# Performance work log

Hardware: AMD Instinct MI355X
Metric: run time of the kernel (lower is better)

Reference implementation:

```python
import jax, jax.numpy as jnp
import numpy as np

N_HEAD = 12
N_EMBD = 768


def setup_inputs() -> dict:
    key = jax.random.key(0)
    k1, k2, k3, k4, k5 = jax.random.split(key, 5)
    B, T, C = 4, 2048, N_EMBD
    s = 0.02
    x = jax.random.normal(k1, (B, T, C), dtype=jnp.float32)
    w_attn = jax.random.normal(k2, (C, 3 * C), dtype=jnp.float32) * s
    b_attn = jnp.zeros((3 * C,), dtype=jnp.float32)
    w_proj = jax.random.normal(k3, (C, C), dtype=jnp.float32) * s
    b_proj = jnp.zeros((C,), dtype=jnp.float32)
    return {"x": x, "w_attn": w_attn, "b_attn": b_attn, "w_proj": w_proj, "b_proj": b_proj}


def reference(x, w_attn, b_attn, w_proj, b_proj):
    # dropout omitted (eval mode / dropout=0.0)
    B, T, C = x.shape
    H = N_HEAD
    D = C // H  # head dim
    qkv = x @ w_attn + b_attn                      # [B,T,3C]
    q, k, v = jnp.split(qkv, 3, axis=-1)
    q = q.reshape(B, T, H, D).transpose(0, 2, 1, 3)  # [B,H,T,D]
    k = k.reshape(B, T, H, D).transpose(0, 2, 1, 3)
    v = v.reshape(B, T, H, D).transpose(0, 2, 1, 3)
    att = jnp.einsum('bhqd,bhkd->bhqk', q, k) * (1.0 / np.sqrt(D))  # [B,H,T,T]
    causal = jnp.tril(jnp.ones((T, T), dtype=bool))
    att = jnp.where(causal[None, None], att, -jnp.inf)
    att = jax.nn.softmax(att, axis=-1)
    y = jnp.einsum('bhqk,bhkd->bhqd', att, v)      # [B,H,T,D]
    y = y.transpose(0, 2, 1, 3).reshape(B, T, C)
    return y @ w_proj + b_proj
```

## Files before the change

### kernel.cpp

```cpp
#include <hip/hip_runtime.h>
#include <stdint.h>

typedef unsigned short ushort_t;

#define T_SEQ 2048
#define BATCH 4
#define NHEAD 12
#define CEMB 768
#define HDIM 64
#define C3 2304

__device__ __forceinline__ ushort_t f2b_hw(float f) {
  union { __bf16 h; ushort_t u; } p;
  p.h = (__bf16)f;
  return p.u;
}
__device__ __forceinline__ uint32_t pkbf16(float lo, float hi) {
  union { __bf16 h[2]; uint32_t u; } p;
  p.h[0] = (__bf16)lo; p.h[1] = (__bf16)hi;
  return p.u;
}

typedef __attribute__((address_space(3))) unsigned int lds_u32_t;
typedef const __attribute__((address_space(1))) unsigned int glb_u32_t;
__device__ __forceinline__ void async_cp16(const void* g, void* l) {
  __builtin_amdgcn_global_load_lds((glb_u32_t*)g, (lds_u32_t*)l, 16, 0, 0);
}

__global__ __launch_bounds__(256) void prep_k(const float* __restrict__ x, ushort_t* __restrict__ xb,
                                              const float* __restrict__ wa, ushort_t* __restrict__ wT,
                                              const float* __restrict__ wp, ushort_t* __restrict__ wpT) {
  const int blk = blockIdx.x;
  const int tid = threadIdx.x;
  if (blk < 3072) {
    const int i = blk * 256 + tid;
    float4 a = ((const float4*)x)[2 * i];
    float4 b = ((const float4*)x)[2 * i + 1];
    uint4 v;
    v.x = pkbf16(a.x, a.y); v.y = pkbf16(a.z, a.w);
    v.z = pkbf16(b.x, b.y); v.w = pkbf16(b.z, b.w);
    ((uint4*)xb)[i] = v;
    return;
  }
  __shared__ ushort_t tile[32][33];
  const float* in; ushort_t* out; int R, C, bx, by;
  if (blk < 4800) {
    const int t = blk - 3072;
    in = wa; out = wT; R = CEMB; C = C3;
    bx = t % 72; by = t / 72;
  } else {
    const int t = blk - 4800;
    in = wp; out = wpT; R = CEMB; C = CEMB;
    bx = t % 24; by = t / 24;
  }
  const int tx = tid & 31, ty = tid >> 5;
  const int c0 = bx * 32, r0 = by * 32;
  for (int i = ty; i < 32; i += 8)
    tile[i][tx] = f2b_hw(in[(size_t)(r0 + i) * C + c0 + tx]);
  __syncthreads();
  for (int i = ty; i < 32; i += 8)
    out[(size_t)(c0 + i) * R + r0 + tx] = tile[tx][i];
}

typedef __bf16 bf16x8 __attribute__((ext_vector_type(8)));
typedef float f32x4 __attribute__((ext_vector_type(4)));

template <bool OUTF, int BM>
__global__ __launch_bounds__(256) void gemm_bt(const ushort_t* __restrict__ A,
                                               const ushort_t* __restrict__ Bt,
                                               const float* __restrict__ bias,
                                               void* __restrict__ Cv,
                                               int M, int N, int K) {
  constexpr int TM = BM / 32;
  __shared__ ushort_t As[2 * BM * 32];
  __shared__ ushort_t Bs[2 * 128 * 32];
  const int tid = threadIdx.x;
  const int m0 = blockIdx.y * BM, n0 = blockIdx.x * 128;
  const int wid = tid >> 6, lane = tid & 63;
  const int quad = lane >> 4, l15 = lane & 15;
  const int wm = (wid >> 1) * (BM / 2), wn = (wid & 1) * 64;
  f32x4 acc[TM][4] = {};

  const int e0 = tid * 8;
  const int r0s = e0 >> 5, c0s = e0 & 31;
  const int e1 = e0 + 2048;
  const int r1s = e1 >> 5, c1s = e1 & 31;

  for (int k0 = 0; k0 < K; k0 += 64) {
    __syncthreads();
#pragma unroll
    for (int p = 0; p < 2; p++) {
      const int kc = k0 + p * 32;
      async_cp16(&A[(size_t)(m0 + r0s) * K + kc + c0s], &As[p * BM * 32 + e0]);
      if constexpr (BM == 128)
        async_cp16(&A[(size_t)(m0 + r1s) * K + kc + c1s], &As[p * BM * 32 + e1]);
      async_cp16(&Bt[(size_t)(n0 + r0s) * K + kc + c0s], &Bs[p * 128 * 32 + e0]);
      async_cp16(&Bt[(size_t)(n0 + r1s) * K + kc + c1s], &Bs[p * 128 * 32 + e1]);
    }
    __syncthreads();
    bf16x8 af[TM][2], bfr[4][2];
#pragma unroll
    for (int t = 0; t < TM; t++)
#pragma unroll
      for (int p = 0; p < 2; p++)
        af[t][p] = *(const bf16x8*)&As[p * BM * 32 + (wm + t * 16 + l15) * 32 + quad * 8];
#pragma unroll
    for (int t = 0; t < 4; t++)
#pragma unroll
      for (int p = 0; p < 2; p++)
        bfr[t][p] = *(const bf16x8*)&Bs[p * 128 * 32 + (wn + t * 16 + l15) * 32 + quad * 8];
#pragma unroll
    for (int p = 0; p < 2; p++)
#pragma unroll
      for (int tm = 0; tm < TM; tm++)
#pragma unroll
        for (int tn = 0; tn < 4; tn++)
          acc[tm][tn] = __builtin_amdgcn_mfma_f32_16x16x32_bf16(af[tm][p], bfr[tn][p], acc[tm][tn], 0, 0, 0);
  }

#pragma unroll
  for (int tm = 0; tm < TM; tm++) {
    const int row = m0 + wm + tm * 16 + quad * 4;
#pragma unroll
    for (int tn = 0; tn < 4; tn++) {
      const int col = n0 + wn + tn * 16 + l15;
      const float bv = bias[col];
#pragma unroll
      for (int rr = 0; rr < 4; rr++) {
        if constexpr (OUTF)
          ((float*)Cv)[(size_t)(row + rr) * N + col] = acc[tm][tn][rr] + bv;
        else
          ((ushort_t*)Cv)[(size_t)(row + rr) * N + col] = f2b_hw(acc[tm][tn][rr] + bv);
      }
    }
  }
}

#define VSTR 64

__device__ __forceinline__ void commit_v(ushort_t* __restrict__ vt, const int* __restrict__ offs,
                                         uint4 pV0, uint4 pV1) {
  union { uint32_t u[4]; uint4 v; } a, c;
  a.v = pV0; c.v = pV1;
#pragma unroll
  for (int j = 0; j < 8; j++) {
    uint32_t pk = __builtin_amdgcn_perm(c.u[j >> 1], a.u[j >> 1],
                                        (j & 1) ? 0x07060302u : 0x05040100u);
    *(uint32_t*)&vt[offs[j]] = pk;
  }
}

__global__ __launch_bounds__(256, 3) void attn_mfma_k(const ushort_t* __restrict__ qkv,
                                                      ushort_t* __restrict__ y) {
  __shared__ ushort_t Ksm[2][2][64 * 32];
  __shared__ ushort_t Vt[2][64 * VSTR];
  __shared__ ushort_t Plds[4][32 * VSTR];

  const int qt = 15 - blockIdx.y;
  const int h = blockIdx.x >> 2, b = blockIdx.x & 3;
  const int tid = threadIdx.x;
  const int w = tid >> 6, lane = tid & 63;
  const int quad = lane >> 4, l15 = lane & 15;
  const int nkt = 2 * qt + 2;
  const int qw = qt * 128 + w * 32;

  const int e0 = tid * 8;
  const int kchunk = (tid & 3) ^ ((tid >> 3) & 3);
  const ushort_t* kbase = qkv + ((size_t)(b * T_SEQ) + (tid >> 2)) * C3 + CEMB + h * HDIM + kchunk * 8;
  const int vpair = tid & 31, vd0 = (tid >> 5) * 8;
  const ushort_t* vbase = qkv + ((size_t)(b * T_SEQ) + 2 * vpair) * C3 + 2 * CEMB + h * HDIM + vd0;
  const size_t step = (size_t)64 * C3;

  int voffw[8];
#pragma unroll
  for (int j = 0; j < 8; j++)
    voffw[j] = (vd0 + j) * VSTR + (((vpair >> 2) ^ j) << 3) + ((vpair & 3) << 1);

  const int sw7 = l15 & 7;
  int koff[4];
#pragma unroll
  for (int m = 0; m < 4; m++)
    koff[m] = (m * 16 + l15) * 32 + ((quad ^ ((l15 >> 1) & 3)) << 3);
  int vroff[2];
#pragma unroll
  for (int kb = 0; kb < 2; kb++)
    vroff[kb] = l15 * VSTR + (((quad + 4 * kb) ^ sw7) << 3);
  int poffW[2][4];
#pragma unroll
  for (int qf = 0; qf < 2; qf++)
#pragma unroll
    for (int m = 0; m < 4; m++)
      poffW[qf][m] = (qf * 16 + l15) * VSTR + (((2 * m + (quad >> 1)) ^ sw7) << 3) + ((quad & 1) << 2);

  const int qrel0 = w * 32 + l15;
  const int qrel1 = qrel0 + 16;

  const float C2 = 0.18033688011112042f;

  bf16x8 qB[2][2];
#pragma unroll
  for (int qf = 0; qf < 2; qf++)
#pragma unroll
    for (int kb = 0; kb < 2; kb++)
      qB[qf][kb] = *(const bf16x8*)&qkv[((size_t)(b * T_SEQ + qw + qf * 16 + l15)) * C3 +
                                        h * HDIM + kb * 32 + quad * 8];

  f32x4 o2[2][4] = {};
  float m0 = -3e38f, m1 = -3e38f;
  float lq0 = 0.f, lq1 = 0.f;

  const ushort_t* kp = kbase;
  const ushort_t* vp = vbase;
  uint4 pV0 = *(const uint4*)vp, pV1 = *(const uint4*)(vp + C3);
  async_cp16(kp, &Ksm[0][0][e0]);
  async_cp16(kp + 32, &Ksm[0][1][e0]);
  commit_v(Vt[0], voffw, pV0, pV1);
  vp += step;
  pV0 = *(const uint4*)vp; pV1 = *(const uint4*)(vp + C3);

  for (int kt = 0; kt < nkt; ++kt) {
    __syncthreads();
    if (kt + 1 < nkt) {
      const int nb = (kt + 1) & 1;
      kp += step;
      async_cp16(kp, &Ksm[nb][0][e0]);
      async_cp16(kp + 32, &Ksm[nb][1][e0]);
      commit_v(Vt[nb], voffw, pV0, pV1);
      if (kt + 2 < nkt) {
        vp += step;
        pV0 = *(const uint4*)vp; pV1 = *(const uint4*)(vp + C3);
      }
    }
    const int cb = kt & 1;

    bf16x8 kA[4][2];
#pragma unroll
    for (int m = 0; m < 4; m++) {
      kA[m][0] = *(const bf16x8*)&Ksm[cb][0][koff[m]];
      kA[m][1] = *(const bf16x8*)&Ksm[cb][1][koff[m]];
    }
    f32x4 st0[4] = {}, st1[4] = {};
#pragma unroll
    for (int m = 0; m < 4; m++) {
      st0[m] = __builtin_amdgcn_mfma_f32_16x16x32_bf16(kA[m][0], qB[0][0], st0[m], 0, 0, 0);
      st0[m] = __builtin_amdgcn_mfma_f32_16x16x32_bf16(kA[m][1], qB[0][1], st0[m], 0, 0, 0);
      st1[m] = __builtin_amdgcn_mfma_f32_16x16x32_bf16(kA[m][0], qB[1][0], st1[m], 0, 0, 0);
      st1[m] = __builtin_amdgcn_mfma_f32_16x16x32_bf16(kA[m][1], qB[1][1], st1[m], 0, 0, 0);
    }

    if (kt >= nkt - 2) {
      const int krel = (kt << 6) - (qt << 7) + quad * 4;
#pragma unroll
      for (int m = 0; m < 4; m++)
#pragma unroll
        for (int r = 0; r < 4; r++) {
          const int kr = krel + m * 16 + r;
          if (kr > qrel0) st0[m][r] = -3e38f;
          if (kr > qrel1) st1[m][r] = -3e38f;
        }
    }

    f32x4 mq0, mq1;
#pragma unroll
    for (int r = 0; r < 4; r++) {
      mq0[r] = fmaxf(fmaxf(st0[0][r], st0[1][r]), fmaxf(st0[2][r], st0[3][r]));
      mq1[r] = fmaxf(fmaxf(st1[0][r], st1[1][r]), fmaxf(st1[2][r], st1[3][r]));
    }
    const float mx0 = fmaxf(fmaxf(mq0[0], mq0[1]), fmaxf(mq0[2], mq0[3]));
    const float mx1 = fmaxf(fmaxf(mq1[0], mq1[1]), fmaxf(mq1[2], mq1[3]));

    float al0 = 1.f, al1 = 1.f;
    const bool viol = (mx0 - m0 > 22.18f) || (mx1 - m1 > 22.18f);
    if (__any(viol)) {
      float a = fmaxf(mx0, __shfl_xor(mx0, 16, 64));
      a = fmaxf(a, __shfl_xor(a, 32, 64));
      float bm = fmaxf(mx1, __shfl_xor(mx1, 16, 64));
      bm = fmaxf(bm, __shfl_xor(bm, 32, 64));
      const float n0 = fmaxf(m0, a), n1 = fmaxf(m1, bm);
      al0 = exp2f((m0 - n0) * C2);
      al1 = exp2f((m1 - n1) * C2);
      m0 = n0; m1 = n1;
#pragma unroll
      for (int nd = 0; nd < 4; nd++)
#pragma unroll
        for (int r = 0; r < 4; r++) {
          o2[0][nd][r] *= al0;
          o2[1][nd][r] *= al1;
        }
    }
    const float mnc0 = m0 * C2, mnc1 = m1 * C2;
#pragma unroll
    for (int m = 0; m < 4; m++)
#pragma unroll
      for (int r = 0; r < 4; r++) {
        st0[m][r] = exp2f(fmaf(st0[m][r], C2, -mnc0));
        st1[m][r] = exp2f(fmaf(st1[m][r], C2, -mnc1));
      }
    f32x4 s40, s41;
#pragma unroll
    for (int r = 0; r < 4; r++) {
      s40[r] = (st0[0][r] + st0[1][r]) + (st0[2][r] + st0[3][r]);
      s41[r] = (st1[0][r] + st1[1][r]) + (st1[2][r] + st1[3][r]);
    }
    lq0 = fmaf(lq0, al0, (s40[0] + s40[1]) + (s40[2] + s40[3]));
    lq1 = fmaf(lq1, al1, (s41[0] + s41[1]) + (s41[2] + s41[3]));

#pragma unroll
    for (int m = 0; m < 4; m++) {
      uint2 pk0, pk1;
      pk0.x = pkbf16(st0[m][0], st0[m][1]);
      pk0.y = pkbf16(st0[m][2], st0[m][3]);
      pk1.x = pkbf16(st1[m][0], st1[m][1]);
      pk1.y = pkbf16(st1[m][2], st1[m][3]);
      *(uint2*)&Plds[w][poffW[0][m]] = pk0;
      *(uint2*)&Plds[w][poffW[1][m]] = pk1;
    }

    asm volatile("s_waitcnt lgkmcnt(0)" ::: "memory");

    bf16x8 ap0[2], ap1[2], bvf[4][2];
#pragma unroll
    for (int kb = 0; kb < 2; kb++) {
      ap0[kb] = *(const bf16x8*)&Plds[w][vroff[kb]];
      ap1[kb] = *(const bf16x8*)&Plds[w][vroff[kb] + 16 * VSTR];
    }
#pragma unroll
    for (int nd = 0; nd < 4; nd++)
#pragma unroll
      for (int kb = 0; kb < 2; kb++)
        bvf[nd][kb] = *(const bf16x8*)&Vt[cb][nd * 1024 + vroff[kb]];
#pragma unroll
    for (int nd = 0; nd < 4; nd++) {
      o2[0][nd] = __builtin_amdgcn_mfma_f32_16x16x32_bf16(bvf[nd][0], ap0[0], o2[0][nd], 0, 0, 0);
      o2[0][nd] = __builtin_amdgcn_mfma_f32_16x16x32_bf16(bvf[nd][1], ap0[1], o2[0][nd], 0, 0, 0);
      o2[1][nd] = __builtin_amdgcn_mfma_f32_16x16x32_bf16(bvf[nd][0], ap1[0], o2[1][nd], 0, 0, 0);
      o2[1][nd] = __builtin_amdgcn_mfma_f32_16x16x32_bf16(bvf[nd][1], ap1[1], o2[1][nd], 0, 0, 0);
    }
  }

  {
    float lt0 = lq0 + __shfl_xor(lq0, 16, 64);
    lt0 += __shfl_xor(lt0, 32, 64);
    float lt1 = lq1 + __shfl_xor(lq1, 16, 64);
    lt1 += __shfl_xor(lt1, 32, 64);
    const float inv0 = 1.0f / lt0, inv1 = 1.0f / lt1;
#pragma unroll
    for (int qf = 0; qf < 2; qf++) {
      const float inv = qf ? inv1 : inv0;
      const int qg = qw + qf * 16 + l15;
      ushort_t* yp = y + ((size_t)(b * T_SEQ + qg)) * CEMB + h * HDIM + quad * 4;
#pragma unroll
      for (int nd = 0; nd < 4; nd++) {
        uint2 pk;
        pk.x = pkbf16(o2[qf][nd][0] * inv, o2[qf][nd][1] * inv);
        pk.y = pkbf16(o2[qf][nd][2] * inv, o2[qf][nd][3] * inv);
        *(uint2*)(yp + nd * 16) = pk;
      }
    }
  }
}

extern "C" void kernel_launch(void* const* d_in, const int* in_sizes, int n_in,
                              void* d_out, int out_size, void* d_ws, size_t ws_size,
                              hipStream_t stream) {
  const float* x      = (const float*)d_in[0];
  const float* w_attn = (const float*)d_in[1];
  const float* b_attn = (const float*)d_in[2];
  const float* w_proj = (const float*)d_in[3];
  const float* b_proj = (const float*)d_in[4];
  float* out = (float*)d_out;

  char* ws = (char*)d_ws;
  ushort_t* qkv = (ushort_t*)ws;
  ushort_t* y   = qkv + (size_t)8192 * 2304;
  ushort_t* xb  = y + (size_t)8192 * 768;
  ushort_t* wT  = xb + (size_t)8192 * 768;
  ushort_t* wpT = wT + (size_t)2304 * 768;

  prep_k<<<5376, 256, 0, stream>>>(x, xb, w_attn, wT, w_proj, wpT);

  gemm_bt<false, 128><<<dim3(C3 / 128, 8192 / 128), 256, 0, stream>>>(xb, wT, b_attn, qkv, 8192, C3, CEMB);

  attn_mfma_k<<<dim3(48, 16), 256, 0, stream>>>(qkv, y);

  gemm_bt<true, 64><<<dim3(CEMB / 128, 8192 / 64), 256, 0, stream>>>(y, wpT, b_proj, out, 8192, CEMB, CEMB);
}
```

Before: 215.9 us.

## Feed P directly from registers into 16x16x16 MFMA, drop P LDS round-trip

Removes the per-wave Plds shared buffer. The softmax probabilities are now packed into bf16 register fragments that already match the B-operand layout of the 16x16x16 MFMA, so they feed the PV product directly with no LDS store, wait and reload. The PV product now issues twice as many smaller MFMAs using 4-element V loads. The change also raises the occupancy hint from 3 to 4 blocks and interleaves query-tile order so heavy and light causal tiles alternate. The trade-off is more MFMA instructions, which have lower per-instruction throughput, and more register pressure under the tighter launch bound.

```diff
diff --git a/kernel.cpp b/kernel.cpp
--- a/kernel.cpp
+++ b/kernel.cpp
@@ -64,6 +64,7 @@
 
 typedef __bf16 bf16x8 __attribute__((ext_vector_type(8)));
 typedef float f32x4 __attribute__((ext_vector_type(4)));
+typedef short short4_t __attribute__((ext_vector_type(4)));
 
 template <bool OUTF, int BM>
 __global__ __launch_bounds__(256) void gemm_bt(const ushort_t* __restrict__ A,
@@ -150,13 +151,13 @@
   }
 }
 
-__global__ __launch_bounds__(256, 3) void attn_mfma_k(const ushort_t* __restrict__ qkv,
+__global__ __launch_bounds__(256, 4) void attn_mfma_k(const ushort_t* __restrict__ qkv,
                                                       ushort_t* __restrict__ y) {
   __shared__ ushort_t Ksm[2][2][64 * 32];
   __shared__ ushort_t Vt[2][64 * VSTR];
-  __shared__ ushort_t Plds[4][32 * VSTR];
-
-  const int qt = 15 - blockIdx.y;
+
+  const int by = blockIdx.y;
+  const int qt = (by & 1) ? (by >> 1) : (15 - (by >> 1));
   const int h = blockIdx.x >> 2, b = blockIdx.x & 3;
   const int tid = threadIdx.x;
   const int w = tid >> 6, lane = tid & 63;
@@ -181,16 +182,13 @@
 #pragma unroll
   for (int m = 0; m < 4; m++)
     koff[m] = (m * 16 + l15) * 32 + ((quad ^ ((l15 >> 1) & 3)) << 3);
-  int vroff[2];
-#pragma unroll
-  for (int kb = 0; kb < 2; kb++)
-    vroff[kb] = l15 * VSTR + (((quad + 4 * kb) ^ sw7) << 3);
-  int poffW[2][4];
-#pragma unroll
-  for (int qf = 0; qf < 2; qf++)
-#pragma unroll
-    for (int m = 0; m < 4; m++)
-      poffW[qf][m] = (qf * 16 + l15) * VSTR + (((2 * m + (quad >> 1)) ^ sw7) << 3) + ((quad & 1) << 2);
+  int vbrow[4], vcm[4];
+#pragma unroll
+  for (int nd = 0; nd < 4; nd++)
+    vbrow[nd] = (nd * 16 + l15) * VSTR + ((quad & 1) << 2);
+#pragma unroll
+  for (int m = 0; m < 4; m++)
+    vcm[m] = ((2 * m + (quad >> 1)) ^ sw7) << 3;
 
   const int qrel0 = w * 32 + l15;
   const int qrel1 = qrel0 + 16;
@@ -305,37 +303,25 @@
     lq0 = fmaf(lq0, al0, (s40[0] + s40[1]) + (s40[2] + s40[3]));
     lq1 = fmaf(lq1, al1, (s41[0] + s41[1]) + (s41[2] + s41[3]));
 
+    short4_t pf0[4], pf1[4];
 #pragma unroll
     for (int m = 0; m < 4; m++) {
-      uint2 pk0, pk1;
-      pk0.x = pkbf16(st0[m][0], st0[m][1]);
-      pk0.y = pkbf16(st0[m][2], st0[m][3]);
-      pk1.x = pkbf16(st1[m][0], st1[m][1]);
-      pk1.y = pkbf16(st1[m][2], st1[m][3]);
-      *(uint2*)&Plds[w][poffW[0][m]] = pk0;
-      *(uint2*)&Plds[w][poffW[1][m]] = pk1;
-    }
-
-    asm volatile("s_waitcnt lgkmcnt(0)" ::: "memory");
-
-    bf16x8 ap0[2], ap1[2], bvf[4][2];
-#pragma unroll
-    for (int kb = 0; kb < 2; kb++) {
-      ap0[kb] = *(const bf16x8*)&Plds[w][vroff[kb]];
-      ap1[kb] = *(const bf16x8*)&Plds[w][vroff[kb] + 16 * VSTR];
-    }
-#pragma unroll
-    for (int nd = 0; nd < 4; nd++)
-#pragma unroll
-      for (int kb = 0; kb < 2; kb++)
-        bvf[nd][kb] = *(const bf16x8*)&Vt[cb][nd * 1024 + vroff[kb]];
-#pragma unroll
-    for (int nd = 0; nd < 4; nd++) {
-      o2[0][nd] = __builtin_amdgcn_mfma_f32_16x16x32_bf16(bvf[nd][0], ap0[0], o2[0][nd], 0, 0, 0);
-      o2[0][nd] = __builtin_amdgcn_mfma_f32_16x16x32_bf16(bvf[nd][1], ap0[1], o2[0][nd], 0, 0, 0);
-      o2[1][nd] = __builtin_amdgcn_mfma_f32_16x16x32_bf16(bvf[nd][0], ap1[0], o2[1][nd], 0, 0, 0);
-      o2[1][nd] = __builtin_amdgcn_mfma_f32_16x16x32_bf16(bvf[nd][1], ap1[1], o2[1][nd], 0, 0, 0);
-    }
+      union { uint32_t u[2]; short4_t s; } pa, pb;
+      pa.u[0] = pkbf16(st0[m][0], st0[m][1]);
+      pa.u[1] = pkbf16(st0[m][2], st0[m][3]);
+      pb.u[0] = pkbf16(st1[m][0], st1[m][1]);
+      pb.u[1] = pkbf16(st1[m][2], st1[m][3]);
+      pf0[m] = pa.s; pf1[m] = pb.s;
+    }
+
+#pragma unroll
+    for (int m = 0; m < 4; m++)
+#pragma unroll
+      for (int nd = 0; nd < 4; nd++) {
+        const short4_t vv = *(const short4_t*)&Vt[cb][vbrow[nd] + vcm[m]];
+        o2[0][nd] = __builtin_amdgcn_mfma_f32_16x16x16bf16_1k(vv, pf0[m], o2[0][nd], 0, 0, 0);
+        o2[1][nd] = __builtin_amdgcn_mfma_f32_16x16x16bf16_1k(vv, pf1[m], o2[1][nd], 0, 0, 0);
+      }
   }
 
   {
```

Result: slower. 239.6 us (+11.0%).
